# Optimization experiments

Hardware: AMD Instinct MI355X
Metric: run time of the kernel (lower is better)

## Reference

```python
import jax, jax.numpy as jnp
import numpy as np

B, T, D, K = 32, 1024, 256, 1024


def setup_inputs() -> dict:
    key = jax.random.key(0)
    k1, k2 = jax.random.split(key)
    z_e_x = jax.random.normal(k1, (B, T, D), dtype=jnp.float32)
    # codebook initialized uniform(-1/K, 1/K) as in VQEmbedding.__init__
    codebook = jax.random.uniform(k2, (K, D), minval=-1.0 / K, maxval=1.0 / K, dtype=jnp.float32)
    return {"z_e_x": z_e_x, "codebook": codebook}


def _vq_indices(x_flat, codebook):
    c_sqr = jnp.sum(codebook * codebook, axis=1)            # [K]
    x_sqr = jnp.sum(x_flat * x_flat, axis=1, keepdims=True)  # [N,1]
    dist = c_sqr[None, :] + x_sqr - 2.0 * (x_flat @ codebook.T)  # [N,K]
    return jnp.argmin(dist, axis=1)                          # [N]


def reference(z_e_x, codebook):
    # VQEmbedding.straight_through with slice=1 (forward values)
    shp = z_e_x.shape
    x_flat = z_e_x.reshape(-1, codebook.shape[1])            # [N,D]
    idx = _vq_indices(x_flat, codebook)                      # [N] int
    codes = codebook[idx].reshape(shp)                       # gather lookup
    # z_q_x and z_q_x_bar are numerically identical (differ only in grad path);
    # also return the indices (what VQEmbedding.forward returns)
    return codes, codes, idx.reshape(shp[:-1])
```

## Files before the change

### kernel.cpp

```cpp
#include <hip/hip_runtime.h>


#define NROWS  32768
#define DDIM   256
#define KCODES 1024
#define MARGIN 1.5e-3f
#define CAP    1024
#define RPB    64
#define NCHUNK 16

typedef __attribute__((ext_vector_type(8))) short short8;
typedef __attribute__((ext_vector_type(4))) float f32x4;

__device__ __forceinline__ unsigned short f2bf(float f) {
    unsigned u = __float_as_uint(f);
    return (unsigned short)((u + 0x7FFFu + ((u >> 16) & 1u)) >> 16);
}

__device__ __forceinline__ float exact_dot(const float* __restrict__ xrow,
                                           const float* __restrict__ crow) {
    const float4* xp = (const float4*)xrow;
    const float4* cp = (const float4*)crow;
    float A = 0.f, B = 0.f;
    #pragma unroll 8
    for (int d4 = 0; d4 < 32; ++d4) {
        float4 xv = xp[d4], cv = cp[d4];
        A = __fmaf_rn(xv.x, cv.x, A);
        A = __fmaf_rn(xv.y, cv.y, A);
        A = __fmaf_rn(xv.z, cv.z, A);
        A = __fmaf_rn(xv.w, cv.w, A);
    }
    #pragma unroll 8
    for (int d4 = 32; d4 < 64; ++d4) {
        float4 xv = xp[d4], cv = cp[d4];
        B = __fmaf_rn(xv.x, cv.x, B);
        B = __fmaf_rn(xv.y, cv.y, B);
        B = __fmaf_rn(xv.z, cv.z, B);
        B = __fmaf_rn(xv.w, cv.w, B);
    }
    return __fadd_rn(A, B);
}

__global__ __launch_bounds__(256) void vq_csqr(const float* __restrict__ cb,
                                               float* __restrict__ csqr) {
    int gid  = blockIdx.x * 256 + threadIdx.x;
    int w    = gid >> 6;
    int lane = threadIdx.x & 63;
    if (w >= KCODES) return;
    float4 v = reinterpret_cast<const float4*>(cb)[w * (DDIM / 4) + lane];
    float s = v.x * v.x + v.y * v.y + v.z * v.z + v.w * v.w;
    #pragma unroll
    for (int off = 32; off > 0; off >>= 1) s += __shfl_down(s, off, 64);
    if (lane == 0) csqr[w] = s;
}

__global__ __launch_bounds__(256) void vq_xsqr(const float* __restrict__ x,
                                               float* __restrict__ xsqr) {
    int w = threadIdx.x >> 6, lane = threadIdx.x & 63;
    int row = blockIdx.x * 4 + w;
    float4 v = reinterpret_cast<const float4*>(x + (size_t)row * DDIM)[lane];
    float s = v.x * v.x + v.y * v.y + v.z * v.z + v.w * v.w;
    #pragma unroll
    for (int off = 32; off > 0; off >>= 1) s += __shfl_down(s, off, 64);
    if (lane == 0) xsqr[row] = s;
}

__global__ __launch_bounds__(256) void vq_cbfrag(const float* __restrict__ cb,
                                                 short* __restrict__ cbh) {
    int id   = blockIdx.x * 256 + threadIdx.x;
    int lane = id & 63;
    int ks   = (id >> 6) & 7;
    int nt   = id >> 9;
    int code = nt * 16 + (lane & 15);
    int d0   = ks * 32 + (lane >> 4) * 8;
    const float4* p = (const float4*)(cb + (size_t)code * DDIM + d0);
    float4 a = p[0], b = p[1];
    short8 v;
    v[0] = (short)f2bf(a.x); v[1] = (short)f2bf(a.y);
    v[2] = (short)f2bf(a.z); v[3] = (short)f2bf(a.w);
    v[4] = (short)f2bf(b.x); v[5] = (short)f2bf(b.y);
    v[6] = (short)f2bf(b.z); v[7] = (short)f2bf(b.w);
    *(short8*)(cbh + (size_t)id * 8) = v;
}

__global__ __launch_bounds__(256, 2) void vq_main(const float* __restrict__ x,
                                                  const float* __restrict__ cb,
                                                  const short* __restrict__ cbh,
                                                  const float* __restrict__ csqr,
                                                  const float* __restrict__ xsqr,
                                                  float* __restrict__ out) {
    __shared__ short              bstage[2][4 * 8 * 64 * 8];
    __shared__ float              csl[KCODES];
    __shared__ float              wred[4][RPB];
    __shared__ float              thrl[RPB];
    __shared__ unsigned long long keys[RPB];
    __shared__ unsigned           list[CAP];
    __shared__ int                fidx[RPB];
    __shared__ int                cnt, ovf;

    const int t    = threadIdx.x;
    const int lane = t & 63;
    const int w    = t >> 6;
    const int r0   = blockIdx.x * RPB;
    const int lr   = lane & 15;
    const int lg   = lane >> 4;

    ((float4*)csl)[t] = ((const float4*)csqr)[t];
    if (t < RPB) keys[t] = ~0ULL;
    if (t == 0) { cnt = 0; ovf = 0; }

    short8 afr[4][8];
    #pragma unroll
    for (int tile = 0; tile < 4; ++tile) {
        const float* xr = x + (size_t)(r0 + tile * 16 + lr) * DDIM;
        #pragma unroll
        for (int ks = 0; ks < 8; ++ks) {
            float4 a = *(const float4*)&xr[ks * 32 + lg * 8];
            float4 b = *(const float4*)&xr[ks * 32 + lg * 8 + 4];
            short8 v;
            v[0] = (short)f2bf(a.x); v[1] = (short)f2bf(a.y);
            v[2] = (short)f2bf(a.z); v[3] = (short)f2bf(a.w);
            v[4] = (short)f2bf(b.x); v[5] = (short)f2bf(b.y);
            v[6] = (short)f2bf(b.z); v[7] = (short)f2bf(b.w);
            afr[tile][ks] = v;
        }
    }

    const char* cbb = (const char*)cbh;
    auto stage_chunk = [&](int buf, int c) {
        const char* srcb = cbb + ((size_t)(w * 16 + c) << 13);
        char*       dstb = (char*)bstage[buf] + ((size_t)w << 13);
        #pragma unroll
        for (int i = 0; i < 8; ++i) {
            const void* src = srcb + i * 1024 + lane * 16;
            __builtin_amdgcn_global_load_lds(
                (const __attribute__((address_space(1))) void*)src,
                (__attribute__((address_space(3))) void*)(dstb + i * 1024),
                16, 0, 0);
        }
    };

    stage_chunk(0, 0);
    __syncthreads();

    float runp[4][4];
    #pragma unroll
    for (int tile = 0; tile < 4; ++tile)
        #pragma unroll
        for (int j = 0; j < 4; ++j) runp[tile][j] = __builtin_inff();
    float thr[4][4];

    for (int cc = 0; cc < 2 * NCHUNK; ++cc) {
        const int c = cc & (NCHUNK - 1);
        if (cc + 1 < 2 * NCHUNK) stage_chunk((cc + 1) & 1, (cc + 1) & (NCHUNK - 1));

        const short* bs = bstage[cc & 1];
        short8 bv[8];
        #pragma unroll
        for (int ks = 0; ks < 8; ++ks)
            bv[ks] = *(const short8*)&bs[((w * 8 + ks) * 64 + lane) * 8];
        f32x4 af[4];
        #pragma unroll
        for (int tile = 0; tile < 4; ++tile) af[tile] = (f32x4){0.f, 0.f, 0.f, 0.f};
        #pragma unroll
        for (int ks = 0; ks < 8; ++ks) {
            #pragma unroll
            for (int tile = 0; tile < 4; ++tile)
                af[tile] = __builtin_amdgcn_mfma_f32_16x16x32_bf16(afr[tile][ks], bv[ks], af[tile], 0, 0, 0);
        }

        const int nt   = w * 16 + c;
        const int code = nt * 16 + lr;
        const float cs1 = __fadd_rn(csl[code], 1.0f);
        if (cc < NCHUNK) {
            #pragma unroll
            for (int tile = 0; tile < 4; ++tile)
                #pragma unroll
                for (int j = 0; j < 4; ++j) {
                    float s = __fmaf_rn(-2.f, af[tile][j], cs1);
                    runp[tile][j] = fminf(runp[tile][j], s);
                }
        } else {
            #pragma unroll
            for (int tile = 0; tile < 4; ++tile)
                #pragma unroll
                for (int j = 0; j < 4; ++j) {
                    float s = __fmaf_rn(-2.f, af[tile][j], cs1);
                    if (s <= thr[tile][j]) {
                        int row = tile * 16 + lg * 4 + j;
                        int pos = atomicAdd(&cnt, 1);
                        if (pos < CAP) list[pos] = ((unsigned)row << 10) | (unsigned)code;
                        else ovf = 1;
                    }
                }
        }

        if (cc == NCHUNK - 1) {
            #pragma unroll
            for (int tile = 0; tile < 4; ++tile)
                #pragma unroll
                for (int j = 0; j < 4; ++j) {
                    float v = runp[tile][j];
                    v = fminf(v, __shfl_xor(v, 1, 64));
                    v = fminf(v, __shfl_xor(v, 2, 64));
                    v = fminf(v, __shfl_xor(v, 4, 64));
                    v = fminf(v, __shfl_xor(v, 8, 64));
                    runp[tile][j] = v;
                }
            if (lr == 0) {
                #pragma unroll
                for (int tile = 0; tile < 4; ++tile)
                    #pragma unroll
                    for (int j = 0; j < 4; ++j)
                        wred[w][tile * 16 + lg * 4 + j] = runp[tile][j];
            }
        }
        __syncthreads();
        if (cc == NCHUNK - 1) {
            if (t < RPB) {
                float m = fminf(fminf(wred[0][t], wred[1][t]), fminf(wred[2][t], wred[3][t]));
                thrl[t] = m + MARGIN;
            }
            __syncthreads();
            #pragma unroll
            for (int tile = 0; tile < 4; ++tile)
                #pragma unroll
                for (int j = 0; j < 4; ++j) thr[tile][j] = thrl[tile * 16 + lg * 4 + j];
        }
    }

    if (ovf || cnt > CAP) {
        for (int it = t; it < RPB * KCODES; it += 256) {
            int row = it >> 10, code = it & (KCODES - 1);
            float dot = exact_dot(x + (size_t)(r0 + row) * DDIM, cb + (size_t)code * DDIM);
            float s   = __fmaf_rn(-2.f, dot, __fadd_rn(csl[code], xsqr[r0 + row]));
            atomicMin(&keys[row], ((unsigned long long)__float_as_uint(s) << 32) | (unsigned)code);
        }
    } else {
        for (int i = t; i < cnt; i += 256) {
            unsigned e = list[i];
            int row = (int)(e >> 10), code = (int)(e & 0x3FFu);
            float dot = exact_dot(x + (size_t)(r0 + row) * DDIM, cb + (size_t)code * DDIM);
            float s   = __fmaf_rn(-2.f, dot, __fadd_rn(csl[code], xsqr[r0 + row]));
            atomicMin(&keys[row], ((unsigned long long)__float_as_uint(s) << 32) | (unsigned)code);
        }
    }
    __syncthreads();

    if (t < RPB) {
        int code = (int)(unsigned)(keys[t] & 0xffffffffu);
        fidx[t] = code;
        out[(size_t)2 * NROWS * DDIM + (r0 + t)] = (float)code;
    }
    __syncthreads();

    const float4* cb4  = (const float4*)cb;
    float4*       out0 = (float4*)out;
    float4*       out1 = out0 + (size_t)NROWS * (DDIM / 4);
    #pragma unroll
    for (int i = 0; i < 16; ++i) {
        int it  = i * 256 + t;
        int row = it >> 6, col = it & 63;
        float4 v = cb4[(size_t)fidx[row] * (DDIM / 4) + col];
        size_t o = (size_t)(r0 + row) * (DDIM / 4) + col;
        out0[o] = v;
        out1[o] = v;
    }
}

extern "C" void kernel_launch(void* const* d_in, const int* in_sizes, int n_in,
                              void* d_out, int out_size, void* d_ws, size_t ws_size,
                              hipStream_t stream) {
    const float* x   = (const float*)d_in[0];
    const float* cb  = (const float*)d_in[1];
    float*       out = (float*)d_out;

    float* ws_csqr = (float*)d_ws;
    float* ws_xsqr = ws_csqr + KCODES;
    short* ws_cbh  = (short*)(ws_xsqr + NROWS);

    vq_cbfrag<<<128,        256, 0, stream>>>(cb, ws_cbh);
    vq_csqr  <<<256,        256, 0, stream>>>(cb, ws_csqr);
    vq_xsqr  <<<NROWS / 4,  256, 0, stream>>>(x, ws_xsqr);
    vq_main  <<<NROWS / RPB, 256, 0, stream>>>(x, cb, ws_cbh, ws_csqr, ws_xsqr, out);
}
```

Before: 101.1 us.

## Load codebook fragments straight to registers and drop cross-wave threshold reduction

Removes the LDS double-buffer staging of the bf16 codebook. Each wave now loads its MFMA B fragments straight from global memory into two register sets that alternate between chunks. The cross-wave min reduction through shared memory is replaced by a per-wave shuffle reduction, which drops the per-chunk __syncthreads barriers. The trade-off is a looser candidate threshold, since each wave only sees its own 256 codes. That can grow the candidate list and trigger the exact-rescoring fallback more often. The extra register buffers also raise VGPR pressure.

After: 123.3 us. 1.22x slower.

```diff
diff --git a/kernel.cpp b/kernel.cpp
--- a/kernel.cpp
+++ b/kernel.cpp
@@ -7,7 +7,6 @@
 #define MARGIN 1.5e-3f
 #define CAP    1024
 #define RPB    64
-#define NCHUNK 16
 
 typedef __attribute__((ext_vector_type(8))) short short8;
 typedef __attribute__((ext_vector_type(4))) float f32x4;
@@ -89,10 +88,7 @@
                                                   const float* __restrict__ csqr,
                                                   const float* __restrict__ xsqr,
                                                   float* __restrict__ out) {
-    __shared__ short              bstage[2][4 * 8 * 64 * 8];
     __shared__ float              csl[KCODES];
-    __shared__ float              wred[4][RPB];
-    __shared__ float              thrl[RPB];
     __shared__ unsigned long long keys[RPB];
     __shared__ unsigned           list[CAP];
     __shared__ int                fidx[RPB];
@@ -108,6 +104,7 @@
     ((float4*)csl)[t] = ((const float4*)csqr)[t];
     if (t < RPB) keys[t] = ~0ULL;
     if (t == 0) { cnt = 0; ovf = 0; }
+    __syncthreads();
 
     short8 afr[4][8];
     #pragma unroll
@@ -126,23 +123,13 @@
         }
     }
 
-    const char* cbb = (const char*)cbh;
-    auto stage_chunk = [&](int buf, int c) {
-        const char* srcb = cbb + ((size_t)(w * 16 + c) << 13);
-        char*       dstb = (char*)bstage[buf] + ((size_t)w << 13);
-        #pragma unroll
-        for (int i = 0; i < 8; ++i) {
-            const void* src = srcb + i * 1024 + lane * 16;
-            __builtin_amdgcn_global_load_lds(
-                (const __attribute__((address_space(1))) void*)src,
-                (__attribute__((address_space(3))) void*)(dstb + i * 1024),
-                16, 0, 0);
-        }
+    const short8* cbh8 = (const short8*)cbh;
+
+    auto load_bv = [&](short8 (&bv)[8], int c) {
+        const short8* bp = cbh8 + (size_t)((w * 16 + c) * 8) * 64 + lane;
+        #pragma unroll
+        for (int ks = 0; ks < 8; ++ks) bv[ks] = bp[(size_t)ks * 64];
     };
-
-    stage_chunk(0, 0);
-    __syncthreads();
-
     float runp[4][4];
     #pragma unroll
     for (int tile = 0; tile < 4; ++tile)
@@ -150,15 +137,7 @@
         for (int j = 0; j < 4; ++j) runp[tile][j] = __builtin_inff();
     float thr[4][4];
 
-    for (int cc = 0; cc < 2 * NCHUNK; ++cc) {
-        const int c = cc & (NCHUNK - 1);
-        if (cc + 1 < 2 * NCHUNK) stage_chunk((cc + 1) & 1, (cc + 1) & (NCHUNK - 1));
-
-        const short* bs = bstage[cc & 1];
-        short8 bv[8];
-        #pragma unroll
-        for (int ks = 0; ks < 8; ++ks)
-            bv[ks] = *(const short8*)&bs[((w * 8 + ks) * 64 + lane) * 8];
+    auto chunk = [&](const short8 (&bv)[8], int c, int pass) {
         f32x4 af[4];
         #pragma unroll
         for (int tile = 0; tile < 4; ++tile) af[tile] = (f32x4){0.f, 0.f, 0.f, 0.f};
@@ -168,18 +147,14 @@
             for (int tile = 0; tile < 4; ++tile)
                 af[tile] = __builtin_amdgcn_mfma_f32_16x16x32_bf16(afr[tile][ks], bv[ks], af[tile], 0, 0, 0);
         }
-
-        const int nt   = w * 16 + c;
-        const int code = nt * 16 + lr;
+        const int code = (w * 16 + c) * 16 + lr;
         const float cs1 = __fadd_rn(csl[code], 1.0f);
-        if (cc < NCHUNK) {
+        if (pass == 1) {
             #pragma unroll
             for (int tile = 0; tile < 4; ++tile)
                 #pragma unroll
-                for (int j = 0; j < 4; ++j) {
-                    float s = __fmaf_rn(-2.f, af[tile][j], cs1);
-                    runp[tile][j] = fminf(runp[tile][j], s);
-                }
+                for (int j = 0; j < 4; ++j)
+                    runp[tile][j] = fminf(runp[tile][j], __fmaf_rn(-2.f, af[tile][j], cs1));
         } else {
             #pragma unroll
             for (int tile = 0; tile < 4; ++tile)
@@ -194,40 +169,35 @@
                     }
                 }
         }
-
-        if (cc == NCHUNK - 1) {
-            #pragma unroll
-            for (int tile = 0; tile < 4; ++tile)
-                #pragma unroll
-                for (int j = 0; j < 4; ++j) {
-                    float v = runp[tile][j];
-                    v = fminf(v, __shfl_xor(v, 1, 64));
-                    v = fminf(v, __shfl_xor(v, 2, 64));
-                    v = fminf(v, __shfl_xor(v, 4, 64));
-                    v = fminf(v, __shfl_xor(v, 8, 64));
-                    runp[tile][j] = v;
-                }
-            if (lr == 0) {
-                #pragma unroll
-                for (int tile = 0; tile < 4; ++tile)
-                    #pragma unroll
-                    for (int j = 0; j < 4; ++j)
-                        wred[w][tile * 16 + lg * 4 + j] = runp[tile][j];
-            }
-        }
-        __syncthreads();
-        if (cc == NCHUNK - 1) {
-            if (t < RPB) {
-                float m = fminf(fminf(wred[0][t], wred[1][t]), fminf(wred[2][t], wred[3][t]));
-                thrl[t] = m + MARGIN;
-            }
-            __syncthreads();
-            #pragma unroll
-            for (int tile = 0; tile < 4; ++tile)
-                #pragma unroll
-                for (int j = 0; j < 4; ++j) thr[tile][j] = thrl[tile * 16 + lg * 4 + j];
-        }
-    }
+    };
+
+    short8 bvA[8], bvB[8];
+    load_bv(bvA, 0);
+    for (int cp = 0; cp < 8; ++cp) {
+        load_bv(bvB, 2 * cp + 1);
+        chunk(bvA, 2 * cp, 1);
+        if (cp < 7) load_bv(bvA, 2 * cp + 2);
+        chunk(bvB, 2 * cp + 1, 1);
+    }
+    #pragma unroll
+    for (int tile = 0; tile < 4; ++tile)
+        #pragma unroll
+        for (int j = 0; j < 4; ++j) {
+            float v = runp[tile][j];
+            v = fminf(v, __shfl_xor(v, 1, 64));
+            v = fminf(v, __shfl_xor(v, 2, 64));
+            v = fminf(v, __shfl_xor(v, 4, 64));
+            v = fminf(v, __shfl_xor(v, 8, 64));
+            thr[tile][j] = v + MARGIN;
+        }
+    load_bv(bvA, 0);
+    for (int cp = 0; cp < 8; ++cp) {
+        load_bv(bvB, 2 * cp + 1);
+        chunk(bvA, 2 * cp, 2);
+        if (cp < 7) load_bv(bvA, 2 * cp + 2);
+        chunk(bvB, 2 * cp + 1, 2);
+    }
+    __syncthreads();
 
     if (ovf || cnt > CAP) {
         for (int it = t; it < RPB * KCODES; it += 256) {
```
